# Kernel optimization log

Measured on AMD Instinct MI355X. Metric: run time of the kernel, lower is better.

Reference implementation:

```python
import jax, jax.numpy as jnp
import numpy as np

B_, L_ = 1, 1024
D_MODEL, D_INNER, D_XB = 2048, 4096, 1024
D_STATE = 16
DT_RANK = 128
INTER = 8192
EPS = 1e-5
GC = D_INNER // D_STATE   # 256 state groups (each covers D_STATE channels)
REP = D_INNER // D_XB     # 4: repeat_kv expansion factor for x and B


def setup_inputs() -> dict:
    key = jax.random.key(0)
    ks = jax.random.split(key, 8)
    s = 0.02
    return {
        "hidden_states": jax.random.normal(ks[0], (B_, L_, D_MODEL), jnp.float32),
        "rms1_w": jnp.ones((D_MODEL,), jnp.float32),
        "in_proj_w": jax.random.normal(ks[1], (2 * D_INNER + 2 * D_XB + DT_RANK, D_MODEL), jnp.float32) * s,
        "dt_proj_w": jax.random.normal(ks[2], (D_INNER, DT_RANK), jnp.float32) * s,
        "dt_proj_b": jax.random.normal(ks[3], (D_INNER,), jnp.float32) * 0.5 - 4.0,
        "A_log": jnp.tile(jnp.log(jnp.arange(1, D_STATE + 1, dtype=jnp.float32)), (D_INNER, 1)),
        "D_skip": jnp.ones((D_INNER,), jnp.float32),
        "out_proj_w": jax.random.normal(ks[4], (D_MODEL, D_INNER), jnp.float32) * s,
        "rms2_w": jnp.ones((D_MODEL,), jnp.float32),
        "gate_w": jax.random.normal(ks[5], (INTER, D_MODEL), jnp.float32) * s,
        "up_w": jax.random.normal(ks[6], (INTER, D_MODEL), jnp.float32) * s,
        "down_w": jax.random.normal(ks[7], (D_MODEL, INTER), jnp.float32) * s,
    }


def _rmsnorm(x, w):
    return x * jax.lax.rsqrt(jnp.mean(x * x, axis=-1, keepdims=True) + EPS) * w


def _mamba(x, in_proj_w, dt_proj_w, dt_proj_b, A_log, D_skip, out_proj_w):
    b, l, _ = x.shape
    zxbcdt = x @ in_proj_w.T  # (b,l, 2*d_inner + 2*d_xb + dt_rank)
    z = zxbcdt[..., :D_INNER]
    xv = zxbcdt[..., D_INNER:D_INNER + D_XB]
    Bm = zxbcdt[..., D_INNER + D_XB:D_INNER + 2 * D_XB]
    Cm = zxbcdt[..., D_INNER + 2 * D_XB:2 * D_INNER + 2 * D_XB]
    dt_in = zxbcdt[..., 2 * D_INNER + 2 * D_XB:]
    dt = jax.nn.softplus(dt_in @ dt_proj_w.T + dt_proj_b)  # (b,l,d_inner)
    # repeat_kv-style expansion of x and B from d_xb to d_inner (grouped by d_state)
    xg = jnp.repeat(xv.reshape(b, l, D_XB // D_STATE, D_STATE), REP, axis=2)  # (b,l,GC,n)
    Bg = jnp.repeat(Bm.reshape(b, l, D_XB // D_STATE, D_STATE), REP, axis=2)  # (b,l,GC,n)
    Cg = Cm.reshape(b, l, GC, D_STATE)                                        # (b,l,GC,n)
    x_full = xg.reshape(b, l, D_INNER)
    A = -jnp.exp(A_log)                       # (d_inner, n)
    dA = jnp.exp(dt[..., None] * A)           # (b,l,d_inner,n)
    dtx = (dt * x_full).reshape(b, l, GC, D_INNER // GC)  # channels per group == D_STATE here
    dBx = (dtx[..., :, None] * Bg[..., None, :]).reshape(b, l, D_INNER, D_STATE)

    def step(h, inp):
        dA_i, dBx_i, C_i = inp
        h = dA_i * h + dBx_i                  # (b,d_inner,n)
        # channel d in group d // D_STATE shares C of that group
        y = jnp.einsum('bgn,bgcn->bgc', C_i, h.reshape(b, GC, D_INNER // GC, D_STATE))
        return h, y.reshape(b, D_INNER)

    h0 = jnp.zeros((b, D_INNER, D_STATE), x.dtype)
    _, ys = jax.lax.scan(step, h0, (dA.transpose(1, 0, 2, 3), dBx.transpose(1, 0, 2, 3), Cg.transpose(1, 0, 2, 3)))
    y = ys.transpose(1, 0, 2) + D_skip * x_full
    y = y * jax.nn.silu(z)
    return y @ out_proj_w.T


def reference(hidden_states, rms1_w, in_proj_w, dt_proj_w, dt_proj_b, A_log, D_skip, out_proj_w, rms2_w, gate_w, up_w, down_w):
    res = hidden_states
    h = _rmsnorm(hidden_states, rms1_w)
    h = res + _mamba(h, in_proj_w, dt_proj_w, dt_proj_b, A_log, D_skip, out_proj_w)
    res = h
    hn = _rmsnorm(h, rms2_w)
    mlp = (jax.nn.silu(hn @ gate_w.T) * (hn @ up_w.T)) @ down_w.T
    return res + mlp
```

## Files before the change

### kernel.cpp

```cpp
#include <hip/hip_runtime.h>
#include <cstdint>
#include <cstddef>

#define L_SEQ   1024
#define DMODEL  2048
#define DINNER  4096
#define DXB     1024
#define DSTATE  16
#define DTRANK  128
#define INTER   8192
#define ZROW    10368
#define NCHUNK  64
#define CLEN    16

typedef __attribute__((ext_vector_type(8))) short  short8;
typedef __attribute__((ext_vector_type(4))) float  floatx4;
typedef unsigned short ushort_t;

__device__ __forceinline__ unsigned short f2bf(float f) {
  unsigned u = __float_as_uint(f);
  u += 0x7FFFu + ((u >> 16) & 1u);
  return (unsigned short)(u >> 16);
}
__device__ __forceinline__ float bf2f(unsigned short h) {
  return __uint_as_float(((unsigned)h) << 16);
}

__device__ __forceinline__ void gl_lds16(const void* g, void* l) {
  __builtin_amdgcn_global_load_lds(
      (const __attribute__((address_space(1))) unsigned int*)g,
      (__attribute__((address_space(3))) unsigned int*)l,
      16, 0, 0);
}

__global__ void __launch_bounds__(256) cvt_kernel(
    const float* __restrict__ src, ushort_t* __restrict__ dst, int n8)
{
  int idx = blockIdx.x * 256 + threadIdx.x;
  if (idx < n8) {
    const float4* s = (const float4*)src + (size_t)idx * 2;
    float4 v0 = s[0], v1 = s[1];
    union { ushort_t u[8]; uint4 v; } o;
    o.u[0] = f2bf(v0.x); o.u[1] = f2bf(v0.y); o.u[2] = f2bf(v0.z); o.u[3] = f2bf(v0.w);
    o.u[4] = f2bf(v1.x); o.u[5] = f2bf(v1.y); o.u[6] = f2bf(v1.z); o.u[7] = f2bf(v1.w);
    ((uint4*)dst)[idx] = o.v;
  }
}

template <int MI, int NI, int EPI, bool WF32>
__global__ void __launch_bounds__(256) gemm_bf16(
    const ushort_t* __restrict__ A, int lda,
    const ushort_t* __restrict__ W, int ldw,
    float* __restrict__ C, int ldc, int K,
    const float* __restrict__ aux,
    ushort_t* __restrict__ Cb, int col_lo, int ldcb)
{
  constexpr int BM = MI * 32, BN = NI * 32;
  constexpr int IA = BM / 64, IB = BN / 64;
  constexpr int ASZ = BM * 32, BSZ = BN * 32;
  __shared__ alignas(16) ushort_t As[2 * ASZ];
  __shared__ alignas(16) ushort_t Bs[2 * BSZ];

  const int kz = blockIdx.z;
  A += (size_t)kz * K;
  W += (size_t)kz * K;
  C += (size_t)kz * gridDim.y * BM * ldc;

  const int m0 = blockIdx.y * BM;
  const int n0 = blockIdx.x * BN;
  const int t = threadIdx.x;
  const int lane = t & 63, wave = t >> 6;
  const int wm = wave & 1, wn = wave >> 1;
  const int lrow = lane & 15, quad = lane >> 4;

  const int srow = wave * 16 + (lane >> 2);
  const int skof = (lane & 3) * 8;

  const ushort_t* gA[IA]; ushort_t* lA[IA];
  const ushort_t* gW[IB]; ushort_t* lB[IB];
#pragma unroll
  for (int j = 0; j < IA; ++j) {
    gA[j] = A + (size_t)(m0 + j * 64 + srow) * lda + skof;
    lA[j] = As + j * 2048 + wave * 512;
  }
#pragma unroll
  for (int j = 0; j < IB; ++j) {
    gW[j] = W + (size_t)(n0 + j * 64 + srow) * ldw + skof;
    lB[j] = Bs + j * 2048 + wave * 512;
  }

  floatx4 zero = {0.f, 0.f, 0.f, 0.f};
  floatx4 acc[MI][NI];
#pragma unroll
  for (int a = 0; a < MI; ++a)
#pragma unroll
    for (int b = 0; b < NI; ++b) acc[a][b] = zero;

#pragma unroll
  for (int j = 0; j < IA; ++j) gl_lds16(gA[j], lA[j]);
#pragma unroll
  for (int j = 0; j < IB; ++j) gl_lds16(gW[j], lB[j]);

  int buf = 0;
  for (int k0 = 0; k0 < K; k0 += 32) {
    __syncthreads();
    const int nk = k0 + 32;
    if (nk < K) {
      const int nb = buf ^ 1;
#pragma unroll
      for (int j = 0; j < IA; ++j) gl_lds16(gA[j] + nk, lA[j] + nb * ASZ);
#pragma unroll
      for (int j = 0; j < IB; ++j) gl_lds16(gW[j] + nk, lB[j] + nb * BSZ);
    }

    short8 af[MI], bf_[NI];
#pragma unroll
    for (int mi = 0; mi < MI; ++mi)
      af[mi] = *(const short8*)&As[buf * ASZ + (wm * (MI * 16) + mi * 16 + lrow) * 32 + quad * 8];
#pragma unroll
    for (int ni = 0; ni < NI; ++ni)
      bf_[ni] = *(const short8*)&Bs[buf * BSZ + (wn * (NI * 16) + ni * 16 + lrow) * 32 + quad * 8];
#pragma unroll
    for (int mi = 0; mi < MI; ++mi)
#pragma unroll
      for (int ni = 0; ni < NI; ++ni)
        acc[mi][ni] = __builtin_amdgcn_mfma_f32_16x16x32_bf16(af[mi], bf_[ni], acc[mi][ni], 0, 0, 0);
    buf ^= 1;
  }

#pragma unroll
  for (int mi = 0; mi < MI; ++mi)
#pragma unroll
    for (int ni = 0; ni < NI; ++ni)
#pragma unroll
      for (int reg = 0; reg < 4; ++reg) {
        int row = m0 + wm * (MI * 16) + mi * 16 + quad * 4 + reg;
        int col = n0 + wn * (NI * 16) + ni * 16 + lrow;
        float v = acc[mi][ni][reg];
        if (EPI == 1) {
          v += aux[col];
          v = (v > 20.f) ? v : log1pf(__expf(v));
        }
        if constexpr (WF32)
          C[(size_t)row * ldc + col] = v;
        if (Cb != nullptr && col >= col_lo)
          Cb[(size_t)row * ldcb + (col - col_lo)] = f2bf(v);
      }
}

template <int S>
__global__ void __launch_bounds__(256) reduce_add_kernel(
    const float* __restrict__ part, int stride4,
    const float* __restrict__ aux, float* __restrict__ out, int n4)
{
  int idx = blockIdx.x * 256 + threadIdx.x;
  if (idx < n4) {
    float4 v = ((const float4*)aux)[idx];
#pragma unroll
    for (int s = 0; s < S; ++s) {
      float4 p = ((const float4*)part)[(size_t)s * stride4 + idx];
      v.x += p.x; v.y += p.y; v.z += p.z; v.w += p.w;
    }
    ((float4*)out)[idx] = v;
  }
}

__global__ void __launch_bounds__(256) reduce_rms_kernel(
    const float* __restrict__ part, int stride,
    const float* __restrict__ hidden,
    const float* __restrict__ w,
    float* __restrict__ h2, ushort_t* __restrict__ hn)
{
  const int row = blockIdx.x;
  const int c0 = threadIdx.x * 8;
  float4 v0 = *(const float4*)(hidden + (size_t)row * DMODEL + c0);
  float4 v1 = *(const float4*)(hidden + (size_t)row * DMODEL + c0 + 4);
#pragma unroll
  for (int s = 0; s < 4; ++s) {
    const float* p = part + (size_t)s * stride + (size_t)row * DMODEL + c0;
    float4 p0 = *(const float4*)p;
    float4 p1 = *(const float4*)(p + 4);
    v0.x += p0.x; v0.y += p0.y; v0.z += p0.z; v0.w += p0.w;
    v1.x += p1.x; v1.y += p1.y; v1.z += p1.z; v1.w += p1.w;
  }
  *(float4*)(h2 + (size_t)row * DMODEL + c0)     = v0;
  *(float4*)(h2 + (size_t)row * DMODEL + c0 + 4) = v1;
  float ss = v0.x*v0.x + v0.y*v0.y + v0.z*v0.z + v0.w*v0.w
           + v1.x*v1.x + v1.y*v1.y + v1.z*v1.z + v1.w*v1.w;
#pragma unroll
  for (int off = 32; off > 0; off >>= 1) ss += __shfl_down(ss, off);
  __shared__ float red[5];
  const int lane = threadIdx.x & 63, wv = threadIdx.x >> 6;
  if (lane == 0) red[wv] = ss;
  __syncthreads();
  if (threadIdx.x == 0)
    red[4] = rsqrtf((red[0] + red[1] + red[2] + red[3]) / (float)DMODEL + 1e-5f);
  __syncthreads();
  const float scale = red[4];
  float4 w0 = *(const float4*)(w + c0);
  float4 w1 = *(const float4*)(w + c0 + 4);
  union { ushort_t u[8]; uint4 q; } o;
  o.u[0] = f2bf(v0.x * scale * w0.x); o.u[1] = f2bf(v0.y * scale * w0.y);
  o.u[2] = f2bf(v0.z * scale * w0.z); o.u[3] = f2bf(v0.w * scale * w0.w);
  o.u[4] = f2bf(v1.x * scale * w1.x); o.u[5] = f2bf(v1.y * scale * w1.y);
  o.u[6] = f2bf(v1.z * scale * w1.z); o.u[7] = f2bf(v1.w * scale * w1.w);
  *(uint4*)(hn + (size_t)row * DMODEL + c0) = o.q;
}

__global__ void __launch_bounds__(256) rmsnorm_kernel(
    const float* __restrict__ x, const float* __restrict__ w,
    ushort_t* __restrict__ out)
{
  const int row = blockIdx.x;
  const float* xr = x + (size_t)row * DMODEL;
  float ss = 0.f;
#pragma unroll
  for (int c = threadIdx.x * 4; c < DMODEL; c += 256 * 4) {
    float4 v = *(const float4*)(xr + c);
    ss += v.x * v.x + v.y * v.y + v.z * v.z + v.w * v.w;
  }
#pragma unroll
  for (int off = 32; off > 0; off >>= 1) ss += __shfl_down(ss, off);
  __shared__ float red[5];
  const int lane = threadIdx.x & 63, wv = threadIdx.x >> 6;
  if (lane == 0) red[wv] = ss;
  __syncthreads();
  if (threadIdx.x == 0)
    red[4] = rsqrtf((red[0] + red[1] + red[2] + red[3]) / (float)DMODEL + 1e-5f);
  __syncthreads();
  const float scale = red[4];
  ushort_t* orow = out + (size_t)row * DMODEL;
#pragma unroll
  for (int c = threadIdx.x * 4; c < DMODEL; c += 256 * 4) {
    float4 v  = *(const float4*)(xr + c);
    float4 w4 = *(const float4*)(w + c);
    ushort4 o;
    o.x = f2bf(v.x * scale * w4.x); o.y = f2bf(v.y * scale * w4.y);
    o.z = f2bf(v.z * scale * w4.z); o.w = f2bf(v.w * scale * w4.w);
    *(ushort4*)(orow + c) = o;
  }
}

__global__ void __launch_bounds__(256) scan_phase1(
    const float* __restrict__ zx, const float* __restrict__ dt,
    const float* __restrict__ A_log,
    float* __restrict__ hend, float* __restrict__ sdtb)
{
  const int gt = blockIdx.x * 256 + threadIdx.x;
  const int i  = gt & 4095;
  const int c  = gt >> 12;
  const int l0 = c * CLEN;

  float a[16];
  *(float4*)&a[0]  = *(const float4*)(A_log + i * 16 + 0);
  *(float4*)&a[4]  = *(const float4*)(A_log + i * 16 + 4);
  *(float4*)&a[8]  = *(const float4*)(A_log + i * 16 + 8);
  *(float4*)&a[12] = *(const float4*)(A_log + i * 16 + 12);
#pragma unroll
  for (int n = 0; n < 16; ++n) a[n] = -__expf(a[n]);

  float h[16];
#pragma unroll
  for (int n = 0; n < 16; ++n) h[n] = 0.f;
  float sdt = 0.f;

  const int xci = DINNER + ((i >> 6) << 4) + (i & 15);
  const int bci = DINNER + DXB + ((i >> 6) << 4);
  const float* zr = zx + (size_t)l0 * ZROW;
  const float* dr = dt + (size_t)l0 * DINNER + i;

#pragma unroll 4
  for (int l = 0; l < CLEN; ++l) {
    const float* row = zr + l * ZROW;
    const float d = dr[l * DINNER];
    const float x = row[xci];
    float B[16];
    *(float4*)&B[0]  = *(const float4*)(row + bci);
    *(float4*)&B[4]  = *(const float4*)(row + bci + 4);
    *(float4*)&B[8]  = *(const float4*)(row + bci + 8);
    *(float4*)&B[12] = *(const float4*)(row + bci + 12);
    sdt += d;
    const float dtx = d * x;
#pragma unroll
    for (int n = 0; n < 16; ++n)
      h[n] = __expf(d * a[n]) * h[n] + dtx * B[n];
  }

  float* he = hend + ((size_t)c * 65536 + i * 16);
  *(float4*)(he + 0)  = *(float4*)&h[0];
  *(float4*)(he + 4)  = *(float4*)&h[4];
  *(float4*)(he + 8)  = *(float4*)&h[8];
  *(float4*)(he + 12) = *(float4*)&h[12];
  sdtb[c * 4096 + i] = sdt;
}

__global__ void __launch_bounds__(256) scan_phase2(
    const float* __restrict__ hend, const float* __restrict__ sdtb,
    const float* __restrict__ A_log,
    float* __restrict__ hstart)
{
  const int cs = blockIdx.x * 256 + threadIdx.x;
  const float a = -__expf(A_log[cs]);
  const int i  = cs >> 4;
  float H = 0.f;
#pragma unroll 8
  for (int c = 0; c < NCHUNK; ++c) {
    hstart[c * 65536 + cs] = H;
    H = __expf(a * sdtb[c * 4096 + i]) * H + hend[c * 65536 + cs];
  }
}

__global__ void __launch_bounds__(256) scan_phase3(
    const float* __restrict__ zx, const float* __restrict__ dt,
    const float* __restrict__ A_log, const float* __restrict__ D_skip,
    const float* __restrict__ hstart,
    ushort_t* __restrict__ y)
{
  const int gt = blockIdx.x * 256 + threadIdx.x;
  const int i  = gt & 4095;
  const int c  = gt >> 12;
  const int l0 = c * CLEN;

  float a[16];
  *(float4*)&a[0]  = *(const float4*)(A_log + i * 16 + 0);
  *(float4*)&a[4]  = *(const float4*)(A_log + i * 16 + 4);
  *(float4*)&a[8]  = *(const float4*)(A_log + i * 16 + 8);
  *(float4*)&a[12] = *(const float4*)(A_log + i * 16 + 12);
#pragma unroll
  for (int n = 0; n < 16; ++n) a[n] = -__expf(a[n]);
  const float dsk = D_skip[i];

  float h[16];
  const float* hs = hstart + ((size_t)c * 65536 + i * 16);
  *(float4*)&h[0]  = *(const float4*)(hs + 0);
  *(float4*)&h[4]  = *(const float4*)(hs + 4);
  *(float4*)&h[8]  = *(const float4*)(hs + 8);
  *(float4*)&h[12] = *(const float4*)(hs + 12);

  const int xci = DINNER + ((i >> 6) << 4) + (i & 15);
  const int bci = DINNER + DXB + ((i >> 6) << 4);
  const int cci = DINNER + 2 * DXB + (i & ~15);
  const float* zr = zx + (size_t)l0 * ZROW;
  const float* dr = dt + (size_t)l0 * DINNER + i;
  ushort_t*    py = y + (size_t)l0 * DINNER + i;

#pragma unroll 2
  for (int l = 0; l < CLEN; ++l) {
    const float* row = zr + l * ZROW;
    const float d = dr[l * DINNER];
    const float x = row[xci];
    const float z = row[i];
    float B[16], C[16];
    *(float4*)&B[0]  = *(const float4*)(row + bci);
    *(float4*)&B[4]  = *(const float4*)(row + bci + 4);
    *(float4*)&B[8]  = *(const float4*)(row + bci + 8);
    *(float4*)&B[12] = *(const float4*)(row + bci + 12);
    *(float4*)&C[0]  = *(const float4*)(row + cci);
    *(float4*)&C[4]  = *(const float4*)(row + cci + 4);
    *(float4*)&C[8]  = *(const float4*)(row + cci + 8);
    *(float4*)&C[12] = *(const float4*)(row + cci + 12);
    const float dtx = d * x;
    float p0 = 0.f, p1 = 0.f, p2 = 0.f, p3 = 0.f;
#pragma unroll
    for (int n = 0; n < 4; ++n) {
      h[n]      = __expf(d * a[n])      * h[n]      + dtx * B[n];
      h[n + 4]  = __expf(d * a[n + 4])  * h[n + 4]  + dtx * B[n + 4];
      h[n + 8]  = __expf(d * a[n + 8])  * h[n + 8]  + dtx * B[n + 8];
      h[n + 12] = __expf(d * a[n + 12]) * h[n + 12] + dtx * B[n + 12];
      p0 += C[n] * h[n];
      p1 += C[n + 4] * h[n + 4];
      p2 += C[n + 8] * h[n + 8];
      p3 += C[n + 12] * h[n + 12];
    }
    const float p = (p0 + p1) + (p2 + p3);
    const float sz = z / (1.f + __expf(-z));
    py[l * DINNER] = f2bf((p + dsk * x) * sz);
  }
}

__global__ void __launch_bounds__(256) silu_mul_kernel(
    const ushort_t* __restrict__ g, const ushort_t* __restrict__ u,
    ushort_t* __restrict__ out, int n8)
{
  const int idx = blockIdx.x * 256 + threadIdx.x;
  if (idx < n8) {
    union { uint4 v; ushort_t u[8]; } gv, uv, ov;
    gv.v = ((const uint4*)g)[idx];
    uv.v = ((const uint4*)u)[idx];
#pragma unroll
    for (int j = 0; j < 8; ++j) {
      float gf = bf2f(gv.u[j]), uf = bf2f(uv.u[j]);
      ov.u[j] = f2bf(gf / (1.f + __expf(-gf)) * uf);
    }
    ((uint4*)out)[idx] = ov.v;
  }
}

extern "C" void kernel_launch(void* const* d_in, const int* in_sizes, int n_in,
                              void* d_out, int out_size, void* d_ws, size_t ws_size,
                              hipStream_t stream)
{
  const float* hidden    = (const float*)d_in[0];
  const float* rms1_w    = (const float*)d_in[1];
  const float* in_proj_w = (const float*)d_in[2];
  const float* dt_proj_w = (const float*)d_in[3];
  const float* dt_proj_b = (const float*)d_in[4];
  const float* A_log     = (const float*)d_in[5];
  const float* D_skip    = (const float*)d_in[6];
  const float* out_proj_w= (const float*)d_in[7];
  const float* rms2_w    = (const float*)d_in[8];
  const float* gate_w    = (const float*)d_in[9];
  const float* up_w      = (const float*)d_in[10];
  const float* down_w    = (const float*)d_in[11];
  float* out = (float*)d_out;

  char* ws = (char*)d_ws;
  ushort_t* h_norm_bf = (ushort_t*)(ws + 0);
  float*    h2        = (float*)   (ws + 4194304);
  ushort_t* hn_bf     = (ushort_t*)(ws + 12582912);
  float*    zxbcdt    = (float*)   (ws + 16777216);
  float*    part1     = (float*)   (ws + 16777216);
  ushort_t* gate_bf   = (ushort_t*)(ws + 16777216);
  ushort_t* up_bf     = (ushort_t*)(ws + 33554432);
  ushort_t* hm_bf     = (ushort_t*)(ws + 50331648);
  float*    dtbuf     = (float*)   (ws + 67108864);
  float*    part2     = (float*)   (ws + 67108864);
  float*    hend_s    = (float*)   (ws + 83886080);
  float*    hstart_s  = (float*)   (ws + 100663296);
  float*    sdtb_s    = (float*)   (ws + 117440512);
  ushort_t* ybuf_bf   = (ushort_t*)(ws + 118489088);
  ushort_t* dtA_bf    = (ushort_t*)(ws + 126877696);
  ushort_t* wbuf      = (ushort_t*)(ws + 127139840);

  rmsnorm_kernel<<<L_SEQ, 256, 0, stream>>>(hidden, rms1_w, h_norm_bf);
  cvt_kernel<<<(ZROW * DMODEL / 8 + 255) / 256, 256, 0, stream>>>(in_proj_w, wbuf, ZROW * DMODEL / 8);
  gemm_bf16<4, 4, 0, true><<<dim3(ZROW / 128, L_SEQ / 128, 1), 256, 0, stream>>>(
      h_norm_bf, DMODEL, wbuf, DMODEL, zxbcdt, ZROW, DMODEL, nullptr,
      dtA_bf, 2 * DINNER + 2 * DXB, DTRANK);
  cvt_kernel<<<(DINNER * DTRANK / 8 + 255) / 256, 256, 0, stream>>>(dt_proj_w, wbuf, DINNER * DTRANK / 8);
  gemm_bf16<2, 4, 1, true><<<dim3(DINNER / 128, L_SEQ / 64, 1), 256, 0, stream>>>(
      dtA_bf, DTRANK, wbuf, DTRANK, dtbuf, DINNER, DTRANK, dt_proj_b,
      nullptr, 0, 0);
  scan_phase1<<<1024, 256, 0, stream>>>(zxbcdt, dtbuf, A_log, hend_s, sdtb_s);
  scan_phase2<<<256, 256, 0, stream>>>(hend_s, sdtb_s, A_log, hstart_s);
  scan_phase3<<<1024, 256, 0, stream>>>(zxbcdt, dtbuf, A_log, D_skip, hstart_s, ybuf_bf);
  cvt_kernel<<<(DMODEL * DINNER / 8 + 255) / 256, 256, 0, stream>>>(out_proj_w, wbuf, DMODEL * DINNER / 8);
  gemm_bf16<2, 4, 0, true><<<dim3(DMODEL / 128, L_SEQ / 64, 4), 256, 0, stream>>>(
      ybuf_bf, DINNER, wbuf, DINNER, part1, DMODEL, DINNER / 4, nullptr,
      nullptr, 0, 0);
  reduce_rms_kernel<<<L_SEQ, 256, 0, stream>>>(
      part1, L_SEQ * DMODEL, hidden, rms2_w, h2, hn_bf);
  cvt_kernel<<<(INTER * DMODEL / 8 + 255) / 256, 256, 0, stream>>>(gate_w, wbuf, INTER * DMODEL / 8);
  gemm_bf16<4, 4, 0, false><<<dim3(INTER / 128, L_SEQ / 128, 1), 256, 0, stream>>>(
      hn_bf, DMODEL, wbuf, DMODEL, nullptr, INTER, DMODEL, nullptr,
      gate_bf, 0, INTER);
  cvt_kernel<<<(INTER * DMODEL / 8 + 255) / 256, 256, 0, stream>>>(up_w, wbuf, INTER * DMODEL / 8);
  gemm_bf16<4, 4, 0, false><<<dim3(INTER / 128, L_SEQ / 128, 1), 256, 0, stream>>>(
      hn_bf, DMODEL, wbuf, DMODEL, nullptr, INTER, DMODEL, nullptr,
      up_bf, 0, INTER);
  silu_mul_kernel<<<(L_SEQ * INTER / 8) / 256, 256, 0, stream>>>(
      gate_bf, up_bf, hm_bf, L_SEQ * INTER / 8);
  cvt_kernel<<<(DMODEL * INTER / 8 + 255) / 256, 256, 0, stream>>>(down_w, wbuf, DMODEL * INTER / 8);
  gemm_bf16<2, 4, 0, true><<<dim3(DMODEL / 128, L_SEQ / 64, 4), 256, 0, stream>>>(
      hm_bf, INTER, wbuf, INTER, part2, DMODEL, INTER / 4, nullptr,
      nullptr, 0, 0);
  reduce_add_kernel<4><<<(L_SEQ * DMODEL / 4) / 256, 256, 0, stream>>>(
      part2, L_SEQ * DMODEL / 4, h2, out, L_SEQ * DMODEL / 4);
}
```

Measured before the change: 680.5 us.

## Convert fp32 weights to bf16 inside GEMM loads and merge gate/up GEMMs

Adds a GEMM variant that loads fp32 weights directly, converts them to bf16 in registers and stores them into LDS. This removes the separate weight conversion passes for dt_proj, out_proj and down_proj, since each GEMM reads its weights only once. The gate and up projections now run as one GEMM over a concatenated bf16 weight buffer, writing an interleaved output that the silu_mul kernel reads back. The grid is also remapped so blockIdx.x walks M. The cost is that the fused path reads weights from global memory into registers instead of using direct LDS loads, which may stall the MFMA loop.

```diff
diff --git a/kernel.cpp b/kernel.cpp
--- a/kernel.cpp
+++ b/kernel.cpp
@@ -47,12 +47,11 @@
   }
 }
 
-template <int MI, int NI, int EPI, bool WF32>
+template <int MI, int NI, bool WF32>
 __global__ void __launch_bounds__(256) gemm_bf16(
     const ushort_t* __restrict__ A, int lda,
     const ushort_t* __restrict__ W, int ldw,
     float* __restrict__ C, int ldc, int K,
-    const float* __restrict__ aux,
     ushort_t* __restrict__ Cb, int col_lo, int ldcb)
 {
   constexpr int BM = MI * 32, BN = NI * 32;
@@ -61,13 +60,8 @@
   __shared__ alignas(16) ushort_t As[2 * ASZ];
   __shared__ alignas(16) ushort_t Bs[2 * BSZ];
 
-  const int kz = blockIdx.z;
-  A += (size_t)kz * K;
-  W += (size_t)kz * K;
-  C += (size_t)kz * gridDim.y * BM * ldc;
-
-  const int m0 = blockIdx.y * BM;
-  const int n0 = blockIdx.x * BN;
+  const int m0 = blockIdx.x * BM;
+  const int n0 = blockIdx.y * BN;
   const int t = threadIdx.x;
   const int lane = t & 63, wave = t >> 6;
   const int wm = wave & 1, wn = wave >> 1;
@@ -126,6 +120,124 @@
       for (int ni = 0; ni < NI; ++ni)
         acc[mi][ni] = __builtin_amdgcn_mfma_f32_16x16x32_bf16(af[mi], bf_[ni], acc[mi][ni], 0, 0, 0);
     buf ^= 1;
+  }
+
+#pragma unroll
+  for (int mi = 0; mi < MI; ++mi)
+#pragma unroll
+    for (int ni = 0; ni < NI; ++ni)
+#pragma unroll
+      for (int reg = 0; reg < 4; ++reg) {
+        int row = m0 + wm * (MI * 16) + mi * 16 + quad * 4 + reg;
+        int col = n0 + wn * (NI * 16) + ni * 16 + lrow;
+        float v = acc[mi][ni][reg];
+        if constexpr (WF32)
+          C[(size_t)row * ldc + col] = v;
+        if (Cb != nullptr && col >= col_lo)
+          Cb[(size_t)row * ldcb + (col - col_lo)] = f2bf(v);
+      }
+}
+
+template <int MI, int NI, int EPI>
+__global__ void __launch_bounds__(256) gemm_skw(
+    const ushort_t* __restrict__ A, int lda,
+    const float* __restrict__ W, int ldw,
+    float* __restrict__ C, int ldc, int K,
+    const float* __restrict__ aux)
+{
+  constexpr int BM = MI * 32, BN = NI * 32;
+  constexpr int IA = BM / 64, IB = BN / 64;
+  constexpr int ASZ = BM * 32, BSZ = BN * 32;
+  __shared__ alignas(16) ushort_t As[2 * ASZ];
+  __shared__ alignas(16) ushort_t Bs[2 * BSZ];
+
+  const int kz = blockIdx.z;
+  A += (size_t)kz * K;
+  W += (size_t)kz * K;
+  C += (size_t)kz * gridDim.x * BM * ldc;
+
+  const int m0 = blockIdx.x * BM;
+  const int n0 = blockIdx.y * BN;
+  const int t = threadIdx.x;
+  const int lane = t & 63, wave = t >> 6;
+  const int wm = wave & 1, wn = wave >> 1;
+  const int lrow = lane & 15, quad = lane >> 4;
+
+  const int srow = wave * 16 + (lane >> 2);
+  const int skof = (lane & 3) * 8;
+
+  const ushort_t* gA[IA]; ushort_t* lA[IA];
+  const float* gW[IB];    ushort_t* swB[IB];
+#pragma unroll
+  for (int j = 0; j < IA; ++j) {
+    gA[j] = A + (size_t)(m0 + j * 64 + srow) * lda + skof;
+    lA[j] = As + j * 2048 + wave * 512;
+  }
+#pragma unroll
+  for (int j = 0; j < IB; ++j) {
+    gW[j] = W + (size_t)(n0 + j * 64 + srow) * ldw + skof;
+    swB[j] = Bs + j * 2048 + wave * 512 + lane * 8;
+  }
+
+  floatx4 zero = {0.f, 0.f, 0.f, 0.f};
+  floatx4 acc[MI][NI];
+#pragma unroll
+  for (int a = 0; a < MI; ++a)
+#pragma unroll
+    for (int b = 0; b < NI; ++b) acc[a][b] = zero;
+
+#pragma unroll
+  for (int j = 0; j < IA; ++j) gl_lds16(gA[j], lA[j]);
+#pragma unroll
+  for (int j = 0; j < IB; ++j) {
+    float w[8];
+    *(float4*)&w[0] = *(const float4*)(gW[j]);
+    *(float4*)&w[4] = *(const float4*)(gW[j] + 4);
+    union { ushort_t u[8]; uint4 q; } p;
+#pragma unroll
+    for (int e = 0; e < 8; ++e) p.u[e] = f2bf(w[e]);
+    *(uint4*)swB[j] = p.q;
+  }
+
+  int buf = 0;
+  for (int k0 = 0; k0 < K; k0 += 32) {
+    __syncthreads();
+    const int nk = k0 + 32;
+    const int nb = buf ^ 1;
+    float wn_[IB][8];
+    if (nk < K) {
+#pragma unroll
+      for (int j = 0; j < IA; ++j) gl_lds16(gA[j] + nk, lA[j] + nb * ASZ);
+#pragma unroll
+      for (int j = 0; j < IB; ++j) {
+        *(float4*)&wn_[j][0] = *(const float4*)(gW[j] + nk);
+        *(float4*)&wn_[j][4] = *(const float4*)(gW[j] + nk + 4);
+      }
+    }
+
+    short8 af[MI], bf_[NI];
+#pragma unroll
+    for (int mi = 0; mi < MI; ++mi)
+      af[mi] = *(const short8*)&As[buf * ASZ + (wm * (MI * 16) + mi * 16 + lrow) * 32 + quad * 8];
+#pragma unroll
+    for (int ni = 0; ni < NI; ++ni)
+      bf_[ni] = *(const short8*)&Bs[buf * BSZ + (wn * (NI * 16) + ni * 16 + lrow) * 32 + quad * 8];
+#pragma unroll
+    for (int mi = 0; mi < MI; ++mi)
+#pragma unroll
+      for (int ni = 0; ni < NI; ++ni)
+        acc[mi][ni] = __builtin_amdgcn_mfma_f32_16x16x32_bf16(af[mi], bf_[ni], acc[mi][ni], 0, 0, 0);
+
+    if (nk < K) {
+#pragma unroll
+      for (int j = 0; j < IB; ++j) {
+        union { ushort_t u[8]; uint4 q; } p;
+#pragma unroll
+        for (int e = 0; e < 8; ++e) p.u[e] = f2bf(wn_[j][e]);
+        *(uint4*)(swB[j] + nb * BSZ) = p.q;
+      }
+    }
+    buf = nb;
   }
 
 #pragma unroll
@@ -141,14 +253,10 @@
           v += aux[col];
           v = (v > 20.f) ? v : log1pf(__expf(v));
         }
-        if constexpr (WF32)
-          C[(size_t)row * ldc + col] = v;
-        if (Cb != nullptr && col >= col_lo)
-          Cb[(size_t)row * ldcb + (col - col_lo)] = f2bf(v);
+        C[(size_t)row * ldc + col] = v;
       }
 }
 
-template <int S>
 __global__ void __launch_bounds__(256) reduce_add_kernel(
     const float* __restrict__ part, int stride4,
     const float* __restrict__ aux, float* __restrict__ out, int n4)
@@ -157,7 +265,7 @@
   if (idx < n4) {
     float4 v = ((const float4*)aux)[idx];
 #pragma unroll
-    for (int s = 0; s < S; ++s) {
+    for (int s = 0; s < 4; ++s) {
       float4 p = ((const float4*)part)[(size_t)s * stride4 + idx];
       v.x += p.x; v.y += p.y; v.z += p.z; v.w += p.w;
     }
@@ -379,14 +487,16 @@
 }
 
 __global__ void __launch_bounds__(256) silu_mul_kernel(
-    const ushort_t* __restrict__ g, const ushort_t* __restrict__ u,
-    ushort_t* __restrict__ out, int n8)
+    const ushort_t* __restrict__ gu, ushort_t* __restrict__ out, int n8)
 {
   const int idx = blockIdx.x * 256 + threadIdx.x;
   if (idx < n8) {
+    const int r  = idx >> 10;
+    const int cc = idx & 1023;
+    const ushort_t* g = gu + (size_t)r * 16384 + cc * 8;
     union { uint4 v; ushort_t u[8]; } gv, uv, ov;
-    gv.v = ((const uint4*)g)[idx];
-    uv.v = ((const uint4*)u)[idx];
+    gv.v = *(const uint4*)g;
+    uv.v = *(const uint4*)(g + 8192);
 #pragma unroll
     for (int j = 0; j < 8; ++j) {
       float gf = bf2f(gv.u[j]), uf = bf2f(uv.u[j]);
@@ -420,8 +530,7 @@
   ushort_t* hn_bf     = (ushort_t*)(ws + 12582912);
   float*    zxbcdt    = (float*)   (ws + 16777216);
   float*    part1     = (float*)   (ws + 16777216);
-  ushort_t* gate_bf   = (ushort_t*)(ws + 16777216);
-  ushort_t* up_bf     = (ushort_t*)(ws + 33554432);
+  ushort_t* gu_bf     = (ushort_t*)(ws + 16777216);
   ushort_t* hm_bf     = (ushort_t*)(ws + 50331648);
   float*    dtbuf     = (float*)   (ws + 67108864);
   float*    part2     = (float*)   (ws + 67108864);
@@ -434,36 +543,27 @@
 
   rmsnorm_kernel<<<L_SEQ, 256, 0, stream>>>(hidden, rms1_w, h_norm_bf);
   cvt_kernel<<<(ZROW * DMODEL / 8 + 255) / 256, 256, 0, stream>>>(in_proj_w, wbuf, ZROW * DMODEL / 8);
-  gemm_bf16<4, 4, 0, true><<<dim3(ZROW / 128, L_SEQ / 128, 1), 256, 0, stream>>>(
-      h_norm_bf, DMODEL, wbuf, DMODEL, zxbcdt, ZROW, DMODEL, nullptr,
+  gemm_bf16<4, 4, true><<<dim3(L_SEQ / 128, ZROW / 128), 256, 0, stream>>>(
+      h_norm_bf, DMODEL, wbuf, DMODEL, zxbcdt, ZROW, DMODEL,
       dtA_bf, 2 * DINNER + 2 * DXB, DTRANK);
-  cvt_kernel<<<(DINNER * DTRANK / 8 + 255) / 256, 256, 0, stream>>>(dt_proj_w, wbuf, DINNER * DTRANK / 8);
-  gemm_bf16<2, 4, 1, true><<<dim3(DINNER / 128, L_SEQ / 64, 1), 256, 0, stream>>>(
-      dtA_bf, DTRANK, wbuf, DTRANK, dtbuf, DINNER, DTRANK, dt_proj_b,
-      nullptr, 0, 0);
+  gemm_skw<2, 4, 1><<<dim3(L_SEQ / 64, DINNER / 128, 1), 256, 0, stream>>>(
+      dtA_bf, DTRANK, dt_proj_w, DTRANK, dtbuf, DINNER, DTRANK, dt_proj_b);
   scan_phase1<<<1024, 256, 0, stream>>>(zxbcdt, dtbuf, A_log, hend_s, sdtb_s);
   scan_phase2<<<256, 256, 0, stream>>>(hend_s, sdtb_s, A_log, hstart_s);
   scan_phase3<<<1024, 256, 0, stream>>>(zxbcdt, dtbuf, A_log, D_skip, hstart_s, ybuf_bf);
-  cvt_kernel<<<(DMODEL * DINNER / 8 + 255) / 256, 256, 0, stream>>>(out_proj_w, wbuf, DMODEL * DINNER / 8);
-  gemm_bf16<2, 4, 0, true><<<dim3(DMODEL / 128, L_SEQ / 64, 4), 256, 0, stream>>>(
-      ybuf_bf, DINNER, wbuf, DINNER, part1, DMODEL, DINNER / 4, nullptr,
-      nullptr, 0, 0);
+  gemm_skw<2, 4, 0><<<dim3(L_SEQ / 64, DMODEL / 128, 4), 256, 0, stream>>>(
+      ybuf_bf, DINNER, out_proj_w, DINNER, part1, DMODEL, DINNER / 4, nullptr);
   reduce_rms_kernel<<<L_SEQ, 256, 0, stream>>>(
       part1, L_SEQ * DMODEL, hidden, rms2_w, h2, hn_bf);
   cvt_kernel<<<(INTER * DMODEL / 8 + 255) / 256, 256, 0, stream>>>(gate_w, wbuf, INTER * DMODEL / 8);
-  gemm_bf16<4, 4, 0, false><<<dim3(INTER / 128, L_SEQ / 128, 1), 256, 0, stream>>>(
-      hn_bf, DMODEL, wbuf, DMODEL, nullptr, INTER, DMODEL, nullptr,
-      gate_bf, 0, INTER);
-  cvt_kernel<<<(INTER * DMODEL / 8 + 255) / 256, 256, 0, stream>>>(up_w, wbuf, INTER * DMODEL / 8);
-  gemm_bf16<4, 4, 0, false><<<dim3(INTER / 128, L_SEQ / 128, 1), 256, 0, stream>>>(
-      hn_bf, DMODEL, wbuf, DMODEL, nullptr, INTER, DMODEL, nullptr,
-      up_bf, 0, INTER);
+  cvt_kernel<<<(INTER * DMODEL / 8 + 255) / 256, 256, 0, stream>>>(up_w, wbuf + (size_t)INTER * DMODEL, INTER * DMODEL / 8);
+  gemm_bf16<4, 4, false><<<dim3(L_SEQ / 128, 2 * INTER / 128), 256, 0, stream>>>(
+      hn_bf, DMODEL, wbuf, DMODEL, nullptr, 0, DMODEL,
+      gu_bf, 0, 2 * INTER);
   silu_mul_kernel<<<(L_SEQ * INTER / 8) / 256, 256, 0, stream>>>(
-      gate_bf, up_bf, hm_bf, L_SEQ * INTER / 8);
-  cvt_kernel<<<(DMODEL * INTER / 8 + 255) / 256, 256, 0, stream>>>(down_w, wbuf, DMODEL * INTER / 8);
-  gemm_bf16<2, 4, 0, true><<<dim3(DMODEL / 128, L_SEQ / 64, 4), 256, 0, stream>>>(
-      hm_bf, INTER, wbuf, INTER, part2, DMODEL, INTER / 4, nullptr,
-      nullptr, 0, 0);
-  reduce_add_kernel<4><<<(L_SEQ * DMODEL / 4) / 256, 256, 0, stream>>>(
+      gu_bf, hm_bf, L_SEQ * INTER / 8);
+  gemm_skw<2, 4, 0><<<dim3(L_SEQ / 64, DMODEL / 128, 4), 256, 0, stream>>>(
+      hm_bf, INTER, down_w, INTER, part2, DMODEL, INTER / 4, nullptr);
+  reduce_add_kernel<<<(L_SEQ * DMODEL / 4) / 256, 256, 0, stream>>>(
       part2, L_SEQ * DMODEL / 4, h2, out, L_SEQ * DMODEL / 4);
 }
```

Result: slower. 735.3 us (+8.0%).
